# Optimization experiments

Hardware: AMD Instinct MI355X
Metric: run time of the kernel (lower is better)

## Reference

```python
import jax, jax.numpy as jnp
import numpy as np

N_NODES = 40000


def _gcn_conv(x, edge_index, W, b):
    """PyG GCNConv: add self-loops, symmetric degree normalization,
    linear transform, gather-scale-scatter aggregation, bias."""
    n = x.shape[0]
    loops = jnp.arange(n, dtype=edge_index.dtype)
    src = jnp.concatenate([edge_index[0], loops])  # [E+N]
    dst = jnp.concatenate([edge_index[1], loops])  # [E+N]
    ones = jnp.ones(src.shape[0], dtype=x.dtype)
    deg = jax.ops.segment_sum(ones, dst, num_segments=n)  # in-degree incl. self-loop
    dinv = jnp.where(deg > 0, jax.lax.rsqrt(deg), 0.0)
    norm = dinv[src] * dinv[dst]  # [E+N]
    h = x @ W  # [n, out]
    msg = h[src] * norm[:, None]  # [E+N, out] gather + scale
    out = jax.ops.segment_sum(msg, dst, num_segments=n)  # scatter-add
    return out + b


def setup_inputs() -> dict:
    key = jax.random.key(0)
    k = jax.random.split(key, 6)
    n, din, dh, dout = N_NODES, 128, 128, 64
    x = jax.random.normal(k[0], (n, din), dtype=jnp.float32)
    edge_index = jax.random.randint(k[1], (2, 640000), 0, n, dtype=jnp.int64)
    W1 = jax.random.normal(k[2], (din, dh), dtype=jnp.float32) / np.sqrt(din)
    b1 = jnp.zeros((dh,), dtype=jnp.float32)
    W2 = jax.random.normal(k[3], (dh, dout), dtype=jnp.float32) / np.sqrt(dh)
    b2 = jnp.zeros((dout,), dtype=jnp.float32)
    return {"x": x, "edge_index": edge_index, "W1": W1, "b1": b1, "W2": W2, "b2": b2}


def reference(x, edge_index, W1, b1, W2, b2):
    h = jax.nn.relu(_gcn_conv(x, edge_index, W1, b1))
    return _gcn_conv(h, edge_index, W2, b2)
```

## Files before the change

### kernel.cpp

```cpp
#include <hip/hip_runtime.h>
#include <hip/hip_fp16.h>


#define N_NODES 40000
#define DIN 128
#define DH 128
#define DOUT 64
#define NEDGES 640000
#define CAP 64

typedef _Float16 f16x8 __attribute__((ext_vector_type(8)));
typedef float f32x4 __attribute__((ext_vector_type(4)));

__global__ void k_init(int* __restrict__ deg, const float* __restrict__ W1,
                       const float* __restrict__ W2,
                       _Float16* __restrict__ WT1, _Float16* __restrict__ WT2, int n) {
    int i = blockIdx.x * 256 + threadIdx.x;
    if (i < n) deg[i] = 0;
    if (i < DIN * DH) {
        int k = i >> 7, nn = i & 127;
        WT1[(size_t)nn * DIN + k] = (_Float16)W1[i];
    }
    if (i < DH * DOUT) {
        int k = i >> 6, nn = i & 63;
        WT2[(size_t)nn * DH + k] = (_Float16)W2[i];
    }
}

__global__ void k_bucket(const int4* __restrict__ src4, const int4* __restrict__ dst4,
                         int* __restrict__ deg, int* __restrict__ ssrc, int E4) {
    int e = blockIdx.x * 256 + threadIdx.x;
    if (e < E4) {
        int4 s = src4[e];
        int4 d = dst4[e];
        int p0 = atomicAdd(&deg[d.x], 1); if (p0 < CAP) ssrc[d.x * CAP + p0] = s.x;
        int p1 = atomicAdd(&deg[d.y], 1); if (p1 < CAP) ssrc[d.y * CAP + p1] = s.y;
        int p2 = atomicAdd(&deg[d.z], 1); if (p2 < CAP) ssrc[d.z * CAP + p2] = s.z;
        int p3 = atomicAdd(&deg[d.w], 1); if (p3 < CAP) ssrc[d.w * CAP + p3] = s.w;
    }
}

__global__ __launch_bounds__(256) void k_gemm1(
    const float* __restrict__ x, const _Float16* __restrict__ WT,
    const int* __restrict__ deg, __half* __restrict__ h)
{
    const int wave = blockIdx.x * 4 + (threadIdx.x >> 6);
    const int lane = threadIdx.x & 63;
    const int m = lane & 15, quad = lane >> 4;

    f32x4 acc[8];
#pragma unroll
    for (int nt = 0; nt < 8; ++nt) acc[nt] = (f32x4){0.f, 0.f, 0.f, 0.f};

    const float* xrow = x + (size_t)(wave * 16 + m) * DIN + quad * 8;
#pragma unroll
    for (int ks = 0; ks < 4; ++ks) {
        float4 xa = *(const float4*)(xrow + ks * 32);
        float4 xb = *(const float4*)(xrow + ks * 32 + 4);
        f16x8 a = { (_Float16)xa.x, (_Float16)xa.y, (_Float16)xa.z, (_Float16)xa.w,
                    (_Float16)xb.x, (_Float16)xb.y, (_Float16)xb.z, (_Float16)xb.w };
#pragma unroll
        for (int nt = 0; nt < 8; ++nt) {
            f16x8 b = *(const f16x8*)(WT + (size_t)(nt * 16 + m) * DIN + ks * 32 + quad * 8);
            acc[nt] = __builtin_amdgcn_mfma_f32_16x16x32_f16(a, b, acc[nt], 0, 0, 0);
        }
    }
#pragma unroll
    for (int r = 0; r < 4; ++r) {
        int orow = wave * 16 + quad * 4 + r;
        float dn = rsqrtf((float)(deg[orow] + 1));
#pragma unroll
        for (int nt = 0; nt < 8; ++nt)
            h[(size_t)orow * DH + nt * 16 + m] = (__half)(acc[nt][r] * dn);
    }
}

__global__ __launch_bounds__(256) void k_agg1(
    const int* __restrict__ deg, const int* __restrict__ ssrc,
    const __half* __restrict__ h, const float* __restrict__ b1,
    __half* __restrict__ x2)
{
    const int node = blockIdx.x * 4 + (threadIdx.x >> 6);
    const int lane = threadIdx.x & 63;
    const __half2* hp = (const __half2*)h;
    const int dg = deg[node];
    const int cnt = min(dg, CAP);
    float2 acc;
    {
        float2 s = __half22float2(hp[(size_t)node * 64 + lane]);
        acc.x = s.x; acc.y = s.y;
    }
    int sv = (lane < cnt) ? ssrc[node * CAP + lane] : 0;
    int e = 0;
    for (; e + 8 <= cnt; e += 8) {
        int s0 = __shfl(sv, e),     s1 = __shfl(sv, e + 1);
        int s2 = __shfl(sv, e + 2), s3 = __shfl(sv, e + 3);
        int s4 = __shfl(sv, e + 4), s5 = __shfl(sv, e + 5);
        int s6 = __shfl(sv, e + 6), s7 = __shfl(sv, e + 7);
        float2 v0 = __half22float2(hp[(size_t)s0 * 64 + lane]);
        float2 v1 = __half22float2(hp[(size_t)s1 * 64 + lane]);
        float2 v2 = __half22float2(hp[(size_t)s2 * 64 + lane]);
        float2 v3 = __half22float2(hp[(size_t)s3 * 64 + lane]);
        float2 v4 = __half22float2(hp[(size_t)s4 * 64 + lane]);
        float2 v5 = __half22float2(hp[(size_t)s5 * 64 + lane]);
        float2 v6 = __half22float2(hp[(size_t)s6 * 64 + lane]);
        float2 v7 = __half22float2(hp[(size_t)s7 * 64 + lane]);
        acc.x += ((v0.x + v1.x) + (v2.x + v3.x)) + ((v4.x + v5.x) + (v6.x + v7.x));
        acc.y += ((v0.y + v1.y) + (v2.y + v3.y)) + ((v4.y + v5.y) + (v6.y + v7.y));
    }
    for (; e < cnt; ++e) {
        int s = __shfl(sv, e);
        float2 v = __half22float2(hp[(size_t)s * 64 + lane]);
        acc.x += v.x; acc.y += v.y;
    }
    const float dn = rsqrtf((float)(dg + 1));
    float vx = dn * acc.x + b1[2 * lane];
    float vy = dn * acc.y + b1[2 * lane + 1];
    __half2 o = __floats2half2_rn(vx > 0.f ? vx : 0.f, vy > 0.f ? vy : 0.f);
    ((__half2*)x2)[(size_t)node * 64 + lane] = o;
}

__global__ __launch_bounds__(256) void k_gemm2(
    const __half* __restrict__ x2, const _Float16* __restrict__ WT,
    const int* __restrict__ deg, __half* __restrict__ h)
{
    const int wave = blockIdx.x * 4 + (threadIdx.x >> 6);
    const int lane = threadIdx.x & 63;
    const int m = lane & 15, quad = lane >> 4;

    f32x4 acc[4];
#pragma unroll
    for (int nt = 0; nt < 4; ++nt) acc[nt] = (f32x4){0.f, 0.f, 0.f, 0.f};

    const _Float16* xrow = (const _Float16*)x2 + (size_t)(wave * 16 + m) * DH + quad * 8;
#pragma unroll
    for (int ks = 0; ks < 4; ++ks) {
        f16x8 a = *(const f16x8*)(xrow + ks * 32);
#pragma unroll
        for (int nt = 0; nt < 4; ++nt) {
            f16x8 b = *(const f16x8*)(WT + (size_t)(nt * 16 + m) * DH + ks * 32 + quad * 8);
            acc[nt] = __builtin_amdgcn_mfma_f32_16x16x32_f16(a, b, acc[nt], 0, 0, 0);
        }
    }
#pragma unroll
    for (int r = 0; r < 4; ++r) {
        int orow = wave * 16 + quad * 4 + r;
        float dn = rsqrtf((float)(deg[orow] + 1));
#pragma unroll
        for (int nt = 0; nt < 4; ++nt)
            h[(size_t)orow * DOUT + nt * 16 + m] = (__half)(acc[nt][r] * dn);
    }
}

__global__ __launch_bounds__(256) void k_agg2(
    const int* __restrict__ deg, const int* __restrict__ ssrc,
    const __half* __restrict__ h, const float* __restrict__ b2,
    float* __restrict__ out)
{
    const int node = blockIdx.x * 4 + (threadIdx.x >> 6);
    const int lane = threadIdx.x & 63;
    const int dg = deg[node];
    const int cnt = min(dg, CAP);
    float acc = (float)h[(size_t)node * 64 + lane];
    int sv = (lane < cnt) ? ssrc[node * CAP + lane] : 0;
    int e = 0;
    for (; e + 8 <= cnt; e += 8) {
        int s0 = __shfl(sv, e),     s1 = __shfl(sv, e + 1);
        int s2 = __shfl(sv, e + 2), s3 = __shfl(sv, e + 3);
        int s4 = __shfl(sv, e + 4), s5 = __shfl(sv, e + 5);
        int s6 = __shfl(sv, e + 6), s7 = __shfl(sv, e + 7);
        float v0 = (float)h[(size_t)s0 * 64 + lane];
        float v1 = (float)h[(size_t)s1 * 64 + lane];
        float v2 = (float)h[(size_t)s2 * 64 + lane];
        float v3 = (float)h[(size_t)s3 * 64 + lane];
        float v4 = (float)h[(size_t)s4 * 64 + lane];
        float v5 = (float)h[(size_t)s5 * 64 + lane];
        float v6 = (float)h[(size_t)s6 * 64 + lane];
        float v7 = (float)h[(size_t)s7 * 64 + lane];
        acc += ((v0 + v1) + (v2 + v3)) + ((v4 + v5) + (v6 + v7));
    }
    for (; e < cnt; ++e) {
        int s = __shfl(sv, e);
        acc += (float)h[(size_t)s * 64 + lane];
    }
    out[(size_t)node * 64 + lane] = rsqrtf((float)(dg + 1)) * acc + b2[lane];
}

extern "C" void kernel_launch(void* const* d_in, const int* in_sizes, int n_in,
                              void* d_out, int out_size, void* d_ws, size_t ws_size,
                              hipStream_t stream) {
    const float* x  = (const float*)d_in[0];
    const int*   ei = (const int*)d_in[1];
    const float* W1 = (const float*)d_in[2];
    const float* b1 = (const float*)d_in[3];
    const float* W2 = (const float*)d_in[4];
    const float* b2 = (const float*)d_in[5];
    float* out = (float*)d_out;

    const int n = N_NODES, E = NEDGES;
    const int* src = ei;
    const int* dst = ei + E;

    char* ws = (char*)d_ws;
    int*      deg  = (int*)(ws + 0);
    _Float16* WT1  = (_Float16*)(ws + 163840);
    _Float16* WT2  = (_Float16*)(ws + 196608);
    int*      ssrc = (int*)(ws + 212992);
    __half*   h1   = (__half*)(ws + 10452992);
    __half*   h2   = (__half*)(ws + 20692992);
    __half*   x2   = (__half*)(ws + 25812992);

    k_init   <<<(n + 255) / 256, 256, 0, stream>>>(deg, W1, W2, WT1, WT2, n);
    k_bucket <<<(E / 4 + 255) / 256, 256, 0, stream>>>((const int4*)src, (const int4*)dst,
                                                       deg, ssrc, E / 4);
    k_gemm1  <<<n / 64, 256, 0, stream>>>(x, WT1, deg, h1);
    k_agg1   <<<n / 4,  256, 0, stream>>>(deg, ssrc, h1, b1, x2);
    k_gemm2  <<<n / 64, 256, 0, stream>>>(x2, WT2, deg, h2);
    k_agg2   <<<n / 4,  256, 0, stream>>>(deg, ssrc, h2, b2, out);
}
```

Measured before the change: 183.0 us.

## Run bucketing alongside GEMM1 and fuse layer-1 aggregation with GEMM2

Puts the edge bucketing and the first GEMM in one launch as disjoint block ranges, so they can run concurrently. Because GEMM1 no longer waits for degrees, the source-side normalization moves into the aggregation, which multiplies each gathered row by a per-edge weight derived from the neighbor's degree. Layer-1 aggregation is fused with the second GEMM through a shared-memory tile of 16 nodes, which removes the x2 round trip and two launches. The cost is extra degree lookups and multiplies per edge, and the inner gather loop is unrolled 4 deep instead of 8.

```diff
diff --git a/kernel.cpp b/kernel.cpp
--- a/kernel.cpp
+++ b/kernel.cpp
@@ -27,128 +27,113 @@
     }
 }
 
-__global__ void k_bucket(const int4* __restrict__ src4, const int4* __restrict__ dst4,
-                         int* __restrict__ deg, int* __restrict__ ssrc, int E4) {
-    int e = blockIdx.x * 256 + threadIdx.x;
-    if (e < E4) {
-        int4 s = src4[e];
-        int4 d = dst4[e];
-        int p0 = atomicAdd(&deg[d.x], 1); if (p0 < CAP) ssrc[d.x * CAP + p0] = s.x;
-        int p1 = atomicAdd(&deg[d.y], 1); if (p1 < CAP) ssrc[d.y * CAP + p1] = s.y;
-        int p2 = atomicAdd(&deg[d.z], 1); if (p2 < CAP) ssrc[d.z * CAP + p2] = s.z;
-        int p3 = atomicAdd(&deg[d.w], 1); if (p3 < CAP) ssrc[d.w * CAP + p3] = s.w;
-    }
-}
-
-__global__ __launch_bounds__(256) void k_gemm1(
+__global__ __launch_bounds__(256) void k_work1(
     const float* __restrict__ x, const _Float16* __restrict__ WT,
-    const int* __restrict__ deg, __half* __restrict__ h)
+    __half* __restrict__ h,
+    const int4* __restrict__ src4, const int4* __restrict__ dst4,
+    int* __restrict__ deg, int* __restrict__ ssrc)
 {
-    const int wave = blockIdx.x * 4 + (threadIdx.x >> 6);
+    if (blockIdx.x < 625) {
+        const int wave = blockIdx.x * 4 + (threadIdx.x >> 6);
+        const int lane = threadIdx.x & 63;
+        const int m = lane & 15, quad = lane >> 4;
+
+        f32x4 acc[8];
+#pragma unroll
+        for (int nt = 0; nt < 8; ++nt) acc[nt] = (f32x4){0.f, 0.f, 0.f, 0.f};
+
+        const float* xrow = x + (size_t)(wave * 16 + m) * DIN + quad * 8;
+#pragma unroll
+        for (int ks = 0; ks < 4; ++ks) {
+            float4 xa = *(const float4*)(xrow + ks * 32);
+            float4 xb = *(const float4*)(xrow + ks * 32 + 4);
+            f16x8 a = { (_Float16)xa.x, (_Float16)xa.y, (_Float16)xa.z, (_Float16)xa.w,
+                        (_Float16)xb.x, (_Float16)xb.y, (_Float16)xb.z, (_Float16)xb.w };
+#pragma unroll
+            for (int nt = 0; nt < 8; ++nt) {
+                f16x8 b = *(const f16x8*)(WT + (size_t)(nt * 16 + m) * DIN + ks * 32 + quad * 8);
+                acc[nt] = __builtin_amdgcn_mfma_f32_16x16x32_f16(a, b, acc[nt], 0, 0, 0);
+            }
+        }
+#pragma unroll
+        for (int r = 0; r < 4; ++r) {
+            int orow = wave * 16 + quad * 4 + r;
+#pragma unroll
+            for (int nt = 0; nt < 8; ++nt)
+                h[(size_t)orow * DH + nt * 16 + m] = (__half)acc[nt][r];
+        }
+    } else {
+        int e = (blockIdx.x - 625) * 256 + threadIdx.x;
+        if (e < NEDGES / 4) {
+            int4 s = src4[e];
+            int4 d = dst4[e];
+            int p0 = atomicAdd(&deg[d.x], 1); if (p0 < CAP) ssrc[d.x * CAP + p0] = s.x;
+            int p1 = atomicAdd(&deg[d.y], 1); if (p1 < CAP) ssrc[d.y * CAP + p1] = s.y;
+            int p2 = atomicAdd(&deg[d.z], 1); if (p2 < CAP) ssrc[d.z * CAP + p2] = s.z;
+            int p3 = atomicAdd(&deg[d.w], 1); if (p3 < CAP) ssrc[d.w * CAP + p3] = s.w;
+        }
+    }
+}
+
+__global__ __launch_bounds__(256) void k_agg1g2(
+    const int* __restrict__ deg, const int* __restrict__ ssrc,
+    const __half* __restrict__ h1, const float* __restrict__ b1,
+    const _Float16* __restrict__ WT2, __half* __restrict__ h2)
+{
+    __shared__ _Float16 xs[16][136];
+    const int w = threadIdx.x >> 6;
     const int lane = threadIdx.x & 63;
+    const int node0 = blockIdx.x * 16;
+    const __half2* hp = (const __half2*)h1;
+
+    for (int i = 0; i < 4; ++i) {
+        const int node = node0 + w * 4 + i;
+        const int dg = deg[node];
+        const int cnt = min(dg, CAP);
+        const float dn = rsqrtf((float)(dg + 1));
+        float2 self = __half22float2(hp[(size_t)node * 64 + lane]);
+        float2 acc = { self.x * dn, self.y * dn };
+        int sv = (lane < cnt) ? ssrc[node * CAP + lane] : 0;
+        float dval = (lane < cnt) ? rsqrtf((float)(deg[sv] + 1)) : 0.f;
+        int e = 0;
+        for (; e + 4 <= cnt; e += 4) {
+            int s0 = __shfl(sv, e),     s1 = __shfl(sv, e + 1);
+            int s2 = __shfl(sv, e + 2), s3 = __shfl(sv, e + 3);
+            float w0 = __shfl(dval, e),     w1 = __shfl(dval, e + 1);
+            float w2 = __shfl(dval, e + 2), w3 = __shfl(dval, e + 3);
+            float2 v0 = __half22float2(hp[(size_t)s0 * 64 + lane]);
+            float2 v1 = __half22float2(hp[(size_t)s1 * 64 + lane]);
+            float2 v2 = __half22float2(hp[(size_t)s2 * 64 + lane]);
+            float2 v3 = __half22float2(hp[(size_t)s3 * 64 + lane]);
+            acc.x += (v0.x * w0 + v1.x * w1) + (v2.x * w2 + v3.x * w3);
+            acc.y += (v0.y * w0 + v1.y * w1) + (v2.y * w2 + v3.y * w3);
+        }
+        for (; e < cnt; ++e) {
+            int s = __shfl(sv, e);
+            float wv = __shfl(dval, e);
+            float2 v = __half22float2(hp[(size_t)s * 64 + lane]);
+            acc.x += v.x * wv; acc.y += v.y * wv;
+        }
+        float vx = dn * acc.x + b1[2 * lane];
+        float vy = dn * acc.y + b1[2 * lane + 1];
+        xs[w * 4 + i][2 * lane]     = (_Float16)(vx > 0.f ? vx : 0.f);
+        xs[w * 4 + i][2 * lane + 1] = (_Float16)(vy > 0.f ? vy : 0.f);
+    }
+    __syncthreads();
+
     const int m = lane & 15, quad = lane >> 4;
-
-    f32x4 acc[8];
-#pragma unroll
-    for (int nt = 0; nt < 8; ++nt) acc[nt] = (f32x4){0.f, 0.f, 0.f, 0.f};
-
-    const float* xrow = x + (size_t)(wave * 16 + m) * DIN + quad * 8;
+    f32x4 acc2 = (f32x4){0.f, 0.f, 0.f, 0.f};
 #pragma unroll
     for (int ks = 0; ks < 4; ++ks) {
-        float4 xa = *(const float4*)(xrow + ks * 32);
-        float4 xb = *(const float4*)(xrow + ks * 32 + 4);
-        f16x8 a = { (_Float16)xa.x, (_Float16)xa.y, (_Float16)xa.z, (_Float16)xa.w,
-                    (_Float16)xb.x, (_Float16)xb.y, (_Float16)xb.z, (_Float16)xb.w };
-#pragma unroll
-        for (int nt = 0; nt < 8; ++nt) {
-            f16x8 b = *(const f16x8*)(WT + (size_t)(nt * 16 + m) * DIN + ks * 32 + quad * 8);
-            acc[nt] = __builtin_amdgcn_mfma_f32_16x16x32_f16(a, b, acc[nt], 0, 0, 0);
-        }
+        f16x8 a = *(const f16x8*)&xs[m][ks * 32 + quad * 8];
+        f16x8 b = *(const f16x8*)(WT2 + (size_t)(w * 16 + m) * DH + ks * 32 + quad * 8);
+        acc2 = __builtin_amdgcn_mfma_f32_16x16x32_f16(a, b, acc2, 0, 0, 0);
     }
 #pragma unroll
     for (int r = 0; r < 4; ++r) {
-        int orow = wave * 16 + quad * 4 + r;
-        float dn = rsqrtf((float)(deg[orow] + 1));
-#pragma unroll
-        for (int nt = 0; nt < 8; ++nt)
-            h[(size_t)orow * DH + nt * 16 + m] = (__half)(acc[nt][r] * dn);
-    }
-}
-
-__global__ __launch_bounds__(256) void k_agg1(
-    const int* __restrict__ deg, const int* __restrict__ ssrc,
-    const __half* __restrict__ h, const float* __restrict__ b1,
-    __half* __restrict__ x2)
-{
-    const int node = blockIdx.x * 4 + (threadIdx.x >> 6);
-    const int lane = threadIdx.x & 63;
-    const __half2* hp = (const __half2*)h;
-    const int dg = deg[node];
-    const int cnt = min(dg, CAP);
-    float2 acc;
-    {
-        float2 s = __half22float2(hp[(size_t)node * 64 + lane]);
-        acc.x = s.x; acc.y = s.y;
-    }
-    int sv = (lane < cnt) ? ssrc[node * CAP + lane] : 0;
-    int e = 0;
-    for (; e + 8 <= cnt; e += 8) {
-        int s0 = __shfl(sv, e),     s1 = __shfl(sv, e + 1);
-        int s2 = __shfl(sv, e + 2), s3 = __shfl(sv, e + 3);
-        int s4 = __shfl(sv, e + 4), s5 = __shfl(sv, e + 5);
-        int s6 = __shfl(sv, e + 6), s7 = __shfl(sv, e + 7);
-        float2 v0 = __half22float2(hp[(size_t)s0 * 64 + lane]);
-        float2 v1 = __half22float2(hp[(size_t)s1 * 64 + lane]);
-        float2 v2 = __half22float2(hp[(size_t)s2 * 64 + lane]);
-        float2 v3 = __half22float2(hp[(size_t)s3 * 64 + lane]);
-        float2 v4 = __half22float2(hp[(size_t)s4 * 64 + lane]);
-        float2 v5 = __half22float2(hp[(size_t)s5 * 64 + lane]);
-        float2 v6 = __half22float2(hp[(size_t)s6 * 64 + lane]);
-        float2 v7 = __half22float2(hp[(size_t)s7 * 64 + lane]);
-        acc.x += ((v0.x + v1.x) + (v2.x + v3.x)) + ((v4.x + v5.x) + (v6.x + v7.x));
-        acc.y += ((v0.y + v1.y) + (v2.y + v3.y)) + ((v4.y + v5.y) + (v6.y + v7.y));
-    }
-    for (; e < cnt; ++e) {
-        int s = __shfl(sv, e);
-        float2 v = __half22float2(hp[(size_t)s * 64 + lane]);
-        acc.x += v.x; acc.y += v.y;
-    }
-    const float dn = rsqrtf((float)(dg + 1));
-    float vx = dn * acc.x + b1[2 * lane];
-    float vy = dn * acc.y + b1[2 * lane + 1];
-    __half2 o = __floats2half2_rn(vx > 0.f ? vx : 0.f, vy > 0.f ? vy : 0.f);
-    ((__half2*)x2)[(size_t)node * 64 + lane] = o;
-}
-
-__global__ __launch_bounds__(256) void k_gemm2(
-    const __half* __restrict__ x2, const _Float16* __restrict__ WT,
-    const int* __restrict__ deg, __half* __restrict__ h)
-{
-    const int wave = blockIdx.x * 4 + (threadIdx.x >> 6);
-    const int lane = threadIdx.x & 63;
-    const int m = lane & 15, quad = lane >> 4;
-
-    f32x4 acc[4];
-#pragma unroll
-    for (int nt = 0; nt < 4; ++nt) acc[nt] = (f32x4){0.f, 0.f, 0.f, 0.f};
-
-    const _Float16* xrow = (const _Float16*)x2 + (size_t)(wave * 16 + m) * DH + quad * 8;
-#pragma unroll
-    for (int ks = 0; ks < 4; ++ks) {
-        f16x8 a = *(const f16x8*)(xrow + ks * 32);
-#pragma unroll
-        for (int nt = 0; nt < 4; ++nt) {
-            f16x8 b = *(const f16x8*)(WT + (size_t)(nt * 16 + m) * DH + ks * 32 + quad * 8);
-            acc[nt] = __builtin_amdgcn_mfma_f32_16x16x32_f16(a, b, acc[nt], 0, 0, 0);
-        }
-    }
-#pragma unroll
-    for (int r = 0; r < 4; ++r) {
-        int orow = wave * 16 + quad * 4 + r;
-        float dn = rsqrtf((float)(deg[orow] + 1));
-#pragma unroll
-        for (int nt = 0; nt < 4; ++nt)
-            h[(size_t)orow * DOUT + nt * 16 + m] = (__half)(acc[nt][r] * dn);
+        int nrow = node0 + quad * 4 + r;
+        float dn = rsqrtf((float)(deg[nrow] + 1));
+        h2[(size_t)nrow * DOUT + w * 16 + m] = (__half)(acc2[r] * dn);
     }
 }
 
@@ -208,13 +193,10 @@
     int*      ssrc = (int*)(ws + 212992);
     __half*   h1   = (__half*)(ws + 10452992);
     __half*   h2   = (__half*)(ws + 20692992);
-    __half*   x2   = (__half*)(ws + 25812992);
 
     k_init   <<<(n + 255) / 256, 256, 0, stream>>>(deg, W1, W2, WT1, WT2, n);
-    k_bucket <<<(E / 4 + 255) / 256, 256, 0, stream>>>((const int4*)src, (const int4*)dst,
-                                                       deg, ssrc, E / 4);
-    k_gemm1  <<<n / 64, 256, 0, stream>>>(x, WT1, deg, h1);
-    k_agg1   <<<n / 4,  256, 0, stream>>>(deg, ssrc, h1, b1, x2);
-    k_gemm2  <<<n / 64, 256, 0, stream>>>(x2, WT2, deg, h2);
+    k_work1  <<<1250, 256, 0, stream>>>(x, WT1, h1, (const int4*)src, (const int4*)dst,
+                                        deg, ssrc);
+    k_agg1g2 <<<n / 16, 256, 0, stream>>>(deg, ssrc, h1, b1, WT2, h2);
     k_agg2   <<<n / 4,  256, 0, stream>>>(deg, ssrc, h2, b2, out);
 }
```

Measured after the change: 181.4 us. No clear change (-0.8%).
